# Performance work log

Measured on AMD Instinct MI355X. Metric: run time of the kernel, lower is better.

## Reference

```python
import jax, jax.numpy as jnp
import numpy as np

B, T, C = 2, 2048, 1024
H = 16
HS = C // H  # 64
FF = 4 * C


def setup_inputs() -> dict:
    key = jax.random.key(0)
    ks = jax.random.split(key, 8)
    s = 0.02
    x = jax.random.normal(ks[0], (B, T, C), dtype=jnp.float32)
    # per-head projection weights, stacked: y = einsum('btc,hcd->bhtd', x, W)
    Wq = jax.random.normal(ks[1], (H, C, HS), dtype=jnp.float32) * s
    Wk = jax.random.normal(ks[2], (H, C, HS), dtype=jnp.float32) * s
    Wv = jax.random.normal(ks[3], (H, C, HS), dtype=jnp.float32) * s
    # nn.Linear weight layout: [out, in]
    Wproj = jax.random.normal(ks[4], (C, H * HS), dtype=jnp.float32) * s
    W1 = jax.random.normal(ks[5], (FF, C), dtype=jnp.float32) * s
    b1 = jnp.zeros((FF,), dtype=jnp.float32)
    W2 = jax.random.normal(ks[6], (C, FF), dtype=jnp.float32) * s
    return {"x": x, "Wq": Wq, "Wk": Wk, "Wv": Wv, "Wproj": Wproj,
            "W1": W1, "b1": b1, "W2": W2}


def reference(x, Wq, Wk, Wv, Wproj, W1, b1, W2):
    Bb, Tt, Cc = x.shape
    # --- multi-head causal self-attention ---
    q = jnp.einsum('btc,hcd->bhtd', x, Wq)
    k = jnp.einsum('btc,hcd->bhtd', x, Wk)
    v = jnp.einsum('btc,hcd->bhtd', x, Wv)
    scale = HS ** (-0.5)
    scores = jnp.einsum('bhtd,bhsd->bhts', q, k) * scale  # [B,H,T,T]
    causal_mask = jnp.triu(jnp.ones((Tt, Tt), dtype=bool), k=1)
    scores = jnp.where(causal_mask, -jnp.inf, scores)
    wei = jax.nn.softmax(scores, axis=-1)
    attn = jnp.einsum('bhts,bhsd->bhtd', wei, v)  # [B,H,T,HS]
    attn = attn.transpose(0, 2, 1, 3).reshape(Bb, Tt, H * HS)  # concat heads
    sa = attn @ Wproj.T  # [B,T,C]
    x = x + sa
    # --- SiLU MLP ---
    h = jax.nn.silu(x @ W1.T + b1)
    x = x + h @ W2.T
    return x
```

## Files before the change

### kernel.cpp

```cpp
#include <hip/hip_runtime.h>

#define BB 2
#define TT 2048
#define CC 1024
#define HH 16
#define HS 64
#define FF 4096
#define MTOK 4096

typedef __attribute__((ext_vector_type(4))) float f32x4;
typedef __attribute__((ext_vector_type(8))) short short8;

__device__ __forceinline__ unsigned short f2b(float f) {
  unsigned int u = __builtin_bit_cast(unsigned int, f);
  u += 0x7fffu + ((u >> 16) & 1u);
  return (unsigned short)(u >> 16);
}

__device__ __forceinline__ float fast_exp2(float x) {
#if __has_builtin(__builtin_amdgcn_exp2f)
  return __builtin_amdgcn_exp2f(x);
#else
  return exp2f(x);
#endif
}

__device__ __forceinline__ unsigned int cvt_pk_bf16(float lo, float hi) {
  unsigned int r;
  asm("v_cvt_pk_bf16_f32 %0, %1, %2" : "=v"(r) : "v"(lo), "v"(hi));
  return r;
}

__global__ void cast_bf16_kernel(const float* __restrict__ src,
                                 unsigned short* __restrict__ dst, int n8) {
  int i = blockIdx.x * 256 + threadIdx.x;
  if (i >= n8) return;
  f32x4 a = reinterpret_cast<const f32x4*>(src)[2 * i];
  f32x4 b = reinterpret_cast<const f32x4*>(src)[2 * i + 1];
  short8 o;
  o[0] = (short)f2b(a[0]); o[1] = (short)f2b(a[1]);
  o[2] = (short)f2b(a[2]); o[3] = (short)f2b(a[3]);
  o[4] = (short)f2b(b[0]); o[5] = (short)f2b(b[1]);
  o[6] = (short)f2b(b[2]); o[7] = (short)f2b(b[3]);
  reinterpret_cast<short8*>(dst)[i] = o;
}

__global__ void prep_wqkv_kernel(const float* __restrict__ wq,
                                 const float* __restrict__ wk,
                                 const float* __restrict__ wv,
                                 unsigned short* __restrict__ dst) {
  __shared__ float tile[64][65];
  const int qkv = blockIdx.y >> 4;
  const int h = blockIdx.y & 15;
  const int c0 = blockIdx.x * 64;
  const float* w = (qkv == 0) ? wq : (qkv == 1) ? wk : wv;
  const float scale = (qkv == 0) ? 0.125f : 1.0f;
  const int dd = threadIdx.x & 63;
  const int rr = threadIdx.x >> 6;
  const float* src = w + ((size_t)h * 1024 + c0) * 64;
#pragma unroll
  for (int it = 0; it < 16; ++it) {
    int c = it * 4 + rr;
    tile[c][dd] = src[(size_t)c * 64 + dd];
  }
  __syncthreads();
  unsigned short* dbase = dst + ((size_t)(qkv * 1024 + h * 64)) * 1024 + c0;
#pragma unroll
  for (int it = 0; it < 16; ++it) {
    int d = it * 4 + rr;
    dbase[(size_t)d * 1024 + dd] = f2b(tile[dd][d] * scale);
  }
}

template <int EPI>
__global__ __launch_bounds__(256, 2) void gemm_bt(
    const unsigned short* __restrict__ A, const unsigned short* __restrict__ Bt,
    const int K, const int N, const float* __restrict__ bias,
    const float* __restrict__ resid, float* __restrict__ outf,
    unsigned short* __restrict__ outb, unsigned short* __restrict__ qout,
    unsigned short* __restrict__ kout, unsigned short* __restrict__ vout) {
  __shared__ __align__(16) unsigned short ldsA[128 * 64];
  __shared__ __align__(16) unsigned short ldsB[128 * 64];
  const int tid = threadIdx.x;
  const int lane = tid & 63;
  const int wave = tid >> 6;
  const int g = lane >> 4, l16 = lane & 15;
  const int wr = wave >> 1, wc = wave & 1;
  const int bm = blockIdx.y, bn = blockIdx.x;

  const int srow = lane >> 3;
  const int schunk = (lane & 7) ^ srow;

  f32x4 acc[4][4] = {};

  const size_t a_row0 = (size_t)bm * 128;
  const size_t b_row0 = (size_t)bn * 128;

  for (int kt = 0; kt < K; kt += 64) {
#pragma unroll
    for (int i = 0; i < 4; ++i) {
      const int row = (wave * 4 + i) * 8 + srow;
      const unsigned short* ga = A + (a_row0 + row) * K + kt + schunk * 8;
      __builtin_amdgcn_global_load_lds(
          (const __attribute__((address_space(1))) unsigned int*)ga,
          (__attribute__((address_space(3))) unsigned int*)(ldsA + (wave * 4 + i) * 512),
          16, 0, 0);
      const unsigned short* gb = Bt + (b_row0 + row) * K + kt + schunk * 8;
      __builtin_amdgcn_global_load_lds(
          (const __attribute__((address_space(1))) unsigned int*)gb,
          (__attribute__((address_space(3))) unsigned int*)(ldsB + (wave * 4 + i) * 512),
          16, 0, 0);
    }
    __syncthreads();
    short8 af[4][2], bfr[4][2];
#pragma unroll
    for (int mi = 0; mi < 4; ++mi)
#pragma unroll
      for (int ks = 0; ks < 2; ++ks) {
        int row = wr * 64 + mi * 16 + l16;
        int ch = (ks * 4 + g) ^ (row & 7);
        af[mi][ks] = *reinterpret_cast<const short8*>(&ldsA[row * 64 + ch * 8]);
      }
#pragma unroll
    for (int ni = 0; ni < 4; ++ni)
#pragma unroll
      for (int ks = 0; ks < 2; ++ks) {
        int row = wc * 64 + ni * 16 + l16;
        int ch = (ks * 4 + g) ^ (row & 7);
        bfr[ni][ks] = *reinterpret_cast<const short8*>(&ldsB[row * 64 + ch * 8]);
      }
#pragma unroll
    for (int ks = 0; ks < 2; ++ks)
#pragma unroll
      for (int mi = 0; mi < 4; ++mi)
#pragma unroll
        for (int ni = 0; ni < 4; ++ni)
          acc[mi][ni] = __builtin_amdgcn_mfma_f32_16x16x32_bf16(
              af[mi][ks], bfr[ni][ks], acc[mi][ni], 0, 0, 0);
    __syncthreads();
  }

#pragma unroll
  for (int mi = 0; mi < 4; ++mi) {
#pragma unroll
    for (int ni = 0; ni < 4; ++ni) {
#pragma unroll
      for (int j = 0; j < 4; ++j) {
        const int row = bm * 128 + wr * 64 + mi * 16 + g * 4 + j;
        const int col = bn * 128 + wc * 64 + ni * 16 + l16;
        float v = acc[mi][ni][j];
        if (EPI == 0) {
          int qkv = col >> 10;
          int hd = col & 1023;
          int h = hd >> 6, d = hd & 63;
          int b = row >> 11, t = row & 2047;
          size_t base = (size_t)(b * HH + h) * (TT * HS);
          if (qkv == 0) {
            qout[base + ((size_t)t << 6) + d] = f2b(v);
          } else if (qkv == 1) {
            size_t off = ((size_t)((t >> 4) * 2 + (d >> 5)) << 9) +
                         ((((d >> 3) & 3) * 16 + (t & 15)) << 3) + (d & 7);
            kout[base + off] = f2b(v);
          } else {
            size_t off = ((size_t)((t >> 6) * 8 + ((d >> 4) << 1) + ((t & 63) >> 5)) << 9) +
                         ((((t >> 3) & 3) * 16 + (d & 15)) << 3) + (t & 7);
            vout[base + off] = f2b(v);
          }
        } else if (EPI == 1) {
          size_t idx = (size_t)row * N + col;
          float r = resid[idx] + v;
          outf[idx] = r;
          outb[idx] = f2b(r);
        } else if (EPI == 2) {
          float pre = v + bias[col];
          float sg = 1.0f / (1.0f + __expf(-pre));
          outb[(size_t)row * N + col] = f2b(pre * sg);
        } else {
          size_t idx = (size_t)row * N + col;
          outf[idx] += v;
        }
      }
    }
  }
}

#define PSTRIDE 66
__global__ __launch_bounds__(256, 4) void attn_fwd(
    const unsigned short* __restrict__ qg, const unsigned short* __restrict__ kg,
    const unsigned short* __restrict__ vtg, unsigned short* __restrict__ att) {
  __shared__ __align__(16) unsigned short plds[4][16 * PSTRIDE];
  __shared__ float olds[4][16][65];
  __shared__ float mlds[4][16], llds[4][16];
  const int lane = threadIdx.x & 63;
  const int wave = threadIdx.x >> 6;
  const int g = lane >> 4, l16 = lane & 15;
  const int bid = blockIdx.x;
  const int bh = (bid & 7) * 4 + ((bid >> 3) & 3);
  const int b = bh >> 4, h = bh & 15;
  const int pi = wave >> 1, split = wave & 1;
  const int pr = (bid >> 5) * 2 + pi;
  const unsigned short* qh = qg + (size_t)bh * (TT * HS);
  const unsigned short* kh = kg + (size_t)bh * (TT * HS);
  const unsigned short* vth = vtg + (size_t)bh * (TT * HS);
  unsigned short* pw = plds[wave];
  const float L2E = 1.4426950408889634f;

  for (int half = 0; half < 2; ++half) {
    const int tile = half ? (127 - pr) : pr;
    const int r0 = tile * 16;

    short8 qf[2];
#pragma unroll
    for (int ks = 0; ks < 2; ++ks)
      qf[ks] = *reinterpret_cast<const short8*>(
          qh + (size_t)(r0 + l16) * 64 + ks * 32 + g * 8);

    f32x4 oacc[4] = {};
    float mrow = -1e30f, lrow = 0.f;

    const int nkt = (r0 + 79) >> 6;
    for (int kt = split; kt < nkt; kt += 2) {
      const int s0 = kt << 6;
      short8 kf[4][2];
#pragma unroll
      for (int ni = 0; ni < 4; ++ni)
#pragma unroll
        for (int ks = 0; ks < 2; ++ks)
          kf[ni][ks] = *reinterpret_cast<const short8*>(
              kh + (((size_t)(kt * 4 + ni) * 2 + ks) << 9) + lane * 8);
      f32x4 s[4] = {};
      __builtin_amdgcn_s_setprio(1);
#pragma unroll
      for (int ks = 0; ks < 2; ++ks)
#pragma unroll
        for (int ni = 0; ni < 4; ++ni)
          s[ni] = __builtin_amdgcn_mfma_f32_16x16x32_bf16(kf[ni][ks], qf[ks],
                                                          s[ni], 0, 0, 0);
      __builtin_amdgcn_s_setprio(0);
      short8 vf[4][2];
#pragma unroll
      for (int dn = 0; dn < 4; ++dn)
#pragma unroll
        for (int ks = 0; ks < 2; ++ks)
          vf[dn][ks] = *reinterpret_cast<const short8*>(
              vth + (((size_t)(kt * 8 + dn * 2 + ks)) << 9) + lane * 8);
      if (kt == nkt - 1) {
        const int sq = r0 + l16;
#pragma unroll
        for (int ni = 0; ni < 4; ++ni)
#pragma unroll
          for (int j = 0; j < 4; ++j) {
            int sk = s0 + ni * 16 + g * 4 + j;
            if (sk > sq) s[ni][j] = -1e30f;
          }
      }
      float t0 = fmaxf(fmaxf(s[0][0], s[0][1]), fmaxf(s[0][2], s[0][3]));
      float t1 = fmaxf(fmaxf(s[1][0], s[1][1]), fmaxf(s[1][2], s[1][3]));
      float t2 = fmaxf(fmaxf(s[2][0], s[2][1]), fmaxf(s[2][2], s[2][3]));
      float t3 = fmaxf(fmaxf(s[3][0], s[3][1]), fmaxf(s[3][2], s[3][3]));
      float cm = fmaxf(fmaxf(t0, t1), fmaxf(t2, t3));
      cm = fmaxf(cm, __shfl_xor(cm, 16));
      cm = fmaxf(cm, __shfl_xor(cm, 32));
      if (__any(cm > mrow + 8.0f)) {
        float mnew = fmaxf(mrow, cm);
        float sc = fast_exp2((mrow - mnew) * L2E);
        mrow = mnew;
        lrow *= sc;
#pragma unroll
        for (int j = 0; j < 4; ++j) {
          float scj = __shfl(sc, g * 4 + j);
#pragma unroll
          for (int dn = 0; dn < 4; ++dn) oacc[dn][j] *= scj;
        }
      }
      const float mL = mrow * L2E;
#pragma unroll
      for (int ni = 0; ni < 4; ++ni)
#pragma unroll
        for (int j = 0; j < 4; ++j)
          s[ni][j] = fast_exp2(__builtin_fmaf(s[ni][j], L2E, -mL));
      float a0 = (s[0][0] + s[0][1]) + (s[0][2] + s[0][3]);
      float a1 = (s[1][0] + s[1][1]) + (s[1][2] + s[1][3]);
      float a2 = (s[2][0] + s[2][1]) + (s[2][2] + s[2][3]);
      float a3 = (s[3][0] + s[3][1]) + (s[3][2] + s[3][3]);
      float ps = (a0 + a1) + (a2 + a3);
      ps += __shfl_xor(ps, 16);
      ps += __shfl_xor(ps, 32);
      lrow += ps;
#pragma unroll
      for (int ni = 0; ni < 4; ++ni) {
        unsigned int w0 = cvt_pk_bf16(s[ni][0], s[ni][1]);
        unsigned int w1 = cvt_pk_bf16(s[ni][2], s[ni][3]);
        unsigned int* pd =
            reinterpret_cast<unsigned int*>(&pw[l16 * PSTRIDE + ni * 16 + g * 4]);
        pd[0] = w0;
        pd[1] = w1;
      }
      asm volatile("" ::: "memory");
      short8 pa[2];
#pragma unroll
      for (int ks = 0; ks < 2; ++ks)
        pa[ks] = *reinterpret_cast<const short8*>(&pw[l16 * PSTRIDE + ks * 32 + g * 8]);
      __builtin_amdgcn_s_setprio(1);
#pragma unroll
      for (int ks = 0; ks < 2; ++ks)
#pragma unroll
        for (int dn = 0; dn < 4; ++dn)
          oacc[dn] = __builtin_amdgcn_mfma_f32_16x16x32_bf16(pa[ks], vf[dn][ks],
                                                             oacc[dn], 0, 0, 0);
      __builtin_amdgcn_s_setprio(0);
      asm volatile("" ::: "memory");
    }
#pragma unroll
    for (int dn = 0; dn < 4; ++dn)
#pragma unroll
      for (int j = 0; j < 4; ++j)
        olds[wave][g * 4 + j][dn * 16 + l16] = oacc[dn][j];
    if (lane < 16) {
      mlds[wave][lane] = mrow;
      llds[wave][lane] = lrow;
    }
    __syncthreads();
    if (split == 0) {
#pragma unroll
      for (int j = 0; j < 4; ++j) {
        const int q = g * 4 + j;
        float mA = mlds[wave][q], lA = llds[wave][q];
        float mB = mlds[wave ^ 1][q], lB = llds[wave ^ 1][q];
        float ms = fmaxf(mA, mB);
        float a = fast_exp2((mA - ms) * L2E);
        float bb = fast_exp2((mB - ms) * L2E);
        float rinv = 1.0f / (lA * a + lB * bb);
        int t = r0 + q;
#pragma unroll
        for (int dn = 0; dn < 4; ++dn) {
          float ob = olds[wave ^ 1][q][dn * 16 + l16];
          float val = (oacc[dn][j] * a + ob * bb) * rinv;
          att[((size_t)(b * TT + t)) * CC + h * 64 + dn * 16 + l16] = f2b(val);
        }
      }
    }
    __syncthreads();
  }
}

extern "C" void kernel_launch(void* const* d_in, const int* in_sizes, int n_in,
                              void* d_out, int out_size, void* d_ws, size_t ws_size,
                              hipStream_t stream) {
  const float* x = (const float*)d_in[0];
  const float* Wq = (const float*)d_in[1];
  const float* Wk = (const float*)d_in[2];
  const float* Wv = (const float*)d_in[3];
  const float* Wproj = (const float*)d_in[4];
  const float* W1 = (const float*)d_in[5];
  const float* b1 = (const float*)d_in[6];
  const float* W2 = (const float*)d_in[7];
  float* out = (float*)d_out;
  char* ws = (char*)d_ws;
  const size_t MB = 1024 * 1024;
  unsigned short* xb = (unsigned short*)(ws + 0 * MB);
  unsigned short* wqkvT = (unsigned short*)(ws + 8 * MB);
  unsigned short* wprojb = (unsigned short*)(ws + 14 * MB);
  unsigned short* w1b = (unsigned short*)(ws + 16 * MB);
  unsigned short* w2b = (unsigned short*)(ws + 24 * MB);
  unsigned short* qb = (unsigned short*)(ws + 32 * MB);
  unsigned short* kpk = (unsigned short*)(ws + 40 * MB);
  unsigned short* vpk = (unsigned short*)(ws + 48 * MB);
  unsigned short* att = (unsigned short*)(ws + 64 * MB);
  unsigned short* x1b = (unsigned short*)(ws + 72 * MB);
  unsigned short* hb = (unsigned short*)(ws + 80 * MB);

  cast_bf16_kernel<<<2048, 256, 0, stream>>>(x, xb, 4194304 / 8);
  cast_bf16_kernel<<<512, 256, 0, stream>>>(Wproj, wprojb, 1048576 / 8);
  cast_bf16_kernel<<<2048, 256, 0, stream>>>(W1, w1b, 4194304 / 8);
  cast_bf16_kernel<<<2048, 256, 0, stream>>>(W2, w2b, 4194304 / 8);
  prep_wqkv_kernel<<<dim3(16, 48), 256, 0, stream>>>(Wq, Wk, Wv, wqkvT);

  gemm_bt<0><<<dim3(24, 32), 256, 0, stream>>>(xb, wqkvT, 1024, 3072, nullptr,
                                               nullptr, nullptr, nullptr, qb, kpk, vpk);
  attn_fwd<<<1024, 256, 0, stream>>>(qb, kpk, vpk, att);
  gemm_bt<1><<<dim3(8, 32), 256, 0, stream>>>(att, wprojb, 1024, 1024, nullptr,
                                              x, out, x1b, nullptr, nullptr, nullptr);
  gemm_bt<2><<<dim3(32, 32), 256, 0, stream>>>(x1b, w1b, 1024, 4096, b1, nullptr,
                                               nullptr, hb, nullptr, nullptr, nullptr);
  gemm_bt<3><<<dim3(8, 32), 256, 0, stream>>>(hb, w2b, 4096, 1024, nullptr, nullptr,
                                              out, nullptr, nullptr, nullptr, nullptr);
  (void)in_sizes; (void)n_in; (void)out_size; (void)ws_size;
}
```

Measured before the change: 242.0 us.

## Split-K the MLP down-projection with a separate reduction, add block swizzle and priority

The final K=4096 GEMM now runs as a 4-way split-K grid. Each slice writes fp32 partials to workspace, and a new reduce kernel sums them into the output. This fixes the under-filled 256-block grid for that GEMM. The change also adds an XCD-aware block-index swizzle to every GEMM, raises launch_bounds occupancy to 4, and brackets the MFMA loop with s_setprio. The cost is 64MB of partial-sum traffic, an extra kernel launch, and possible register pressure from the higher occupancy hint.

```diff
diff --git a/kernel.cpp b/kernel.cpp
--- a/kernel.cpp
+++ b/kernel.cpp
@@ -72,8 +72,19 @@
   }
 }
 
+__global__ void reduce4_kernel(const float* __restrict__ p, float* __restrict__ out) {
+  const size_t i = (size_t)blockIdx.x * 256 + threadIdx.x;
+  const size_t S = (size_t)1 << 20;
+  f32x4 a = reinterpret_cast<const f32x4*>(p)[i];
+  f32x4 b = reinterpret_cast<const f32x4*>(p)[i + S];
+  f32x4 c = reinterpret_cast<const f32x4*>(p)[i + 2 * S];
+  f32x4 d = reinterpret_cast<const f32x4*>(p)[i + 3 * S];
+  f32x4 o = reinterpret_cast<f32x4*>(out)[i];
+  reinterpret_cast<f32x4*>(out)[i] = o + ((a + b) + (c + d));
+}
+
 template <int EPI>
-__global__ __launch_bounds__(256, 2) void gemm_bt(
+__global__ __launch_bounds__(256, 4) void gemm_bt(
     const unsigned short* __restrict__ A, const unsigned short* __restrict__ Bt,
     const int K, const int N, const float* __restrict__ bias,
     const float* __restrict__ resid, float* __restrict__ outf,
@@ -86,7 +97,18 @@
   const int wave = tid >> 6;
   const int g = lane >> 4, l16 = lane & 15;
   const int wr = wave >> 1, wc = wave & 1;
-  const int bm = blockIdx.y, bn = blockIdx.x;
+
+  const int gx = gridDim.x;
+  const int nwg = gx * gridDim.y;
+  const int lid = blockIdx.y * gx + blockIdx.x;
+  const int qch = nwg >> 3;
+  const int swz = (lid & 7) * qch + (lid >> 3);
+  const int bm = swz / gx;
+  const int bn = swz % gx;
+
+  const int kspan = K / gridDim.z;
+  const int klo = blockIdx.z * kspan;
+  const int khi = klo + kspan;
 
   const int srow = lane >> 3;
   const int schunk = (lane & 7) ^ srow;
@@ -96,7 +118,7 @@
   const size_t a_row0 = (size_t)bm * 128;
   const size_t b_row0 = (size_t)bn * 128;
 
-  for (int kt = 0; kt < K; kt += 64) {
+  for (int kt = klo; kt < khi; kt += 64) {
 #pragma unroll
     for (int i = 0; i < 4; ++i) {
       const int row = (wave * 4 + i) * 8 + srow;
@@ -129,6 +151,7 @@
         int ch = (ks * 4 + g) ^ (row & 7);
         bfr[ni][ks] = *reinterpret_cast<const short8*>(&ldsB[row * 64 + ch * 8]);
       }
+    __builtin_amdgcn_s_setprio(1);
 #pragma unroll
     for (int ks = 0; ks < 2; ++ks)
 #pragma unroll
@@ -137,6 +160,7 @@
         for (int ni = 0; ni < 4; ++ni)
           acc[mi][ni] = __builtin_amdgcn_mfma_f32_16x16x32_bf16(
               af[mi][ks], bfr[ni][ks], acc[mi][ni], 0, 0, 0);
+    __builtin_amdgcn_s_setprio(0);
     __syncthreads();
   }
 
@@ -176,8 +200,7 @@
           float sg = 1.0f / (1.0f + __expf(-pre));
           outb[(size_t)row * N + col] = f2b(pre * sg);
         } else {
-          size_t idx = (size_t)row * N + col;
-          outf[idx] += v;
+          outf[((size_t)blockIdx.z << 22) + (size_t)row * N + col] = v;
         }
       }
     }
@@ -362,13 +385,14 @@
   unsigned short* wqkvT = (unsigned short*)(ws + 8 * MB);
   unsigned short* wprojb = (unsigned short*)(ws + 14 * MB);
   unsigned short* w1b = (unsigned short*)(ws + 16 * MB);
-  unsigned short* w2b = (unsigned short*)(ws + 24 * MB);
   unsigned short* qb = (unsigned short*)(ws + 32 * MB);
   unsigned short* kpk = (unsigned short*)(ws + 40 * MB);
   unsigned short* vpk = (unsigned short*)(ws + 48 * MB);
-  unsigned short* att = (unsigned short*)(ws + 64 * MB);
-  unsigned short* x1b = (unsigned short*)(ws + 72 * MB);
-  unsigned short* hb = (unsigned short*)(ws + 80 * MB);
+  unsigned short* att = (unsigned short*)(ws + 56 * MB);
+  unsigned short* x1b = (unsigned short*)(ws + 64 * MB);
+  unsigned short* hb = (unsigned short*)(ws + 72 * MB);
+  unsigned short* w2b = (unsigned short*)(ws + 104 * MB);
+  float* mlp2p = (float*)(ws + 0 * MB);
 
   cast_bf16_kernel<<<2048, 256, 0, stream>>>(x, xb, 4194304 / 8);
   cast_bf16_kernel<<<512, 256, 0, stream>>>(Wproj, wprojb, 1048576 / 8);
@@ -383,7 +407,8 @@
                                               x, out, x1b, nullptr, nullptr, nullptr);
   gemm_bt<2><<<dim3(32, 32), 256, 0, stream>>>(x1b, w1b, 1024, 4096, b1, nullptr,
                                                nullptr, hb, nullptr, nullptr, nullptr);
-  gemm_bt<3><<<dim3(8, 32), 256, 0, stream>>>(hb, w2b, 4096, 1024, nullptr, nullptr,
-                                              out, nullptr, nullptr, nullptr, nullptr);
+  gemm_bt<3><<<dim3(8, 32, 4), 256, 0, stream>>>(hb, w2b, 4096, 1024, nullptr, nullptr,
+                                                 mlp2p, nullptr, nullptr, nullptr, nullptr);
+  reduce4_kernel<<<4096, 256, 0, stream>>>(mlp2p, out);
   (void)in_sizes; (void)n_in; (void)out_size; (void)ws_size;
 }
```

After: 414.9 us. 1.71x slower.
